# Performance work log

Measured on AMD Instinct MI355X. Metric: run time of the kernel, lower is better.

Reference implementation:

```python
import jax, jax.numpy as jnp
import numpy as np

C = 192          # channels
HEADS = 4        # num_heads
HID = int(C * 2.66)  # 510, GDFN hidden features
B, H, W = 2, 192, 192


def setup_inputs() -> dict:
    key = jax.random.key(0)
    ks = jax.random.split(key, 8)
    def nrm(k, shape, scale=0.02):
        return jax.random.normal(k, shape, jnp.float32) * scale
    return dict(
        x=jax.random.normal(ks[0], (B, C, H, W), jnp.float32),
        qkv_w=nrm(ks[1], (3 * C, C)),
        qkv_b=jnp.zeros((3 * C,), jnp.float32),
        qkv_dw_w=nrm(ks[2], (3 * C, 1, 3, 3)),
        qkv_dw_b=jnp.zeros((3 * C,), jnp.float32),
        attn_out_w=nrm(ks[3], (C, C)),
        attn_out_b=jnp.zeros((C,), jnp.float32),
        temperature=jnp.ones((HEADS, 1, 1), jnp.float32),
        proj_in_w=nrm(ks[4], (2 * HID, C)),
        proj_in_b=jnp.zeros((2 * HID,), jnp.float32),
        dw_w=nrm(ks[5], (2 * HID, 1, 3, 3)),
        dw_b=jnp.zeros((2 * HID,), jnp.float32),
        proj_out_w=nrm(ks[6], (C, HID)),
        proj_out_b=jnp.zeros((C,), jnp.float32),
    )


def _instance_norm(x):
    # torch InstanceNorm2d default: affine=False, eps=1e-5, biased var over spatial dims
    m = x.mean(axis=(2, 3), keepdims=True)
    v = ((x - m) ** 2).mean(axis=(2, 3), keepdims=True)
    return (x - m) * jax.lax.rsqrt(v + 1e-5)


def _conv1x1(x, w, b):
    return jnp.einsum('oc,bchw->bohw', w, x) + b[None, :, None, None]


def _dwconv3x3(x, w, b):
    y = jax.lax.conv_general_dilated(
        x, w, window_strides=(1, 1), padding='SAME',
        feature_group_count=x.shape[1],
        dimension_numbers=('NCHW', 'OIHW', 'NCHW'))
    return y + b[None, :, None, None]


def _l2norm(x, eps=1e-12):
    # F.normalize(dim=-1)
    n = jnp.sqrt(jnp.sum(x * x, axis=-1, keepdims=True))
    return x / jnp.maximum(n, eps)


def reference(x, qkv_w, qkv_b, qkv_dw_w, qkv_dw_b, attn_out_w, attn_out_b,
              temperature, proj_in_w, proj_in_b, dw_w, dw_b, proj_out_w, proj_out_b):
    b, c, h, w = x.shape
    hw = h * w
    dh = c // HEADS  # per-head channel dim

    # --- transposed (channel) attention branch ---
    y = _instance_norm(x)
    qkv = _dwconv3x3(_conv1x1(y, qkv_w, qkv_b), qkv_dw_w, qkv_dw_b)  # [b, 3c, h, w]
    q, k, v = jnp.split(qkv, 3, axis=1)
    q = _l2norm(q.reshape(b, HEADS, dh, hw))  # normalize along spatial dim
    k = _l2norm(k.reshape(b, HEADS, dh, hw))
    v = v.reshape(b, HEADS, dh, hw)
    attn = jnp.einsum('bhcn,bhdn->bhcd', q, k) * temperature  # small [b,heads,dh,dh]
    attn = jax.nn.softmax(attn, axis=-1)
    out = jnp.einsum('bhcd,bhdn->bhcn', attn, v).reshape(b, c, h, w)
    x = x + _conv1x1(out, attn_out_w, attn_out_b)

    # --- gated depthwise FFN (GDFN) branch ---
    y = _instance_norm(x)
    y = _dwconv3x3(_conv1x1(y, proj_in_w, proj_in_b), dw_w, dw_b)  # [b, 2*HID, h, w]
    y1, y2 = jnp.split(y, 2, axis=1)
    y = _conv1x1(jax.nn.gelu(y1, approximate=False) * y2, proj_out_w, proj_out_b)
    return x + y
```

## Files before the change

kernel.cpp:

```cpp
#include <hip/hip_runtime.h>
#include <math.h>

#define HW 36864
#define IMGW 192

typedef unsigned short u16;
typedef __attribute__((ext_vector_type(8))) short short8;
typedef __attribute__((ext_vector_type(8))) unsigned short ushort8;
typedef __attribute__((ext_vector_type(16))) float f32x16;

__device__ __forceinline__ float b2f(u16 u){ return __uint_as_float(((unsigned)u)<<16); }
__device__ __forceinline__ u16 f2b(float f){
    unsigned u = __float_as_uint(f);
    return (u16)((u + 0x7FFFu + ((u>>16)&1u)) >> 16);
}
__device__ __forceinline__ int perm1020(int m){ return (m&1) ? 510+(m>>1) : (m>>1); }
__device__ __forceinline__ int rot2(int ch){ return ((ch<<2)|(ch>>3)) & 31; }
__device__ __forceinline__ float gelu_exact(float x){
    return 0.5f * x * (1.f + erff(x * 0.70710678118654752f));
}
__device__ __forceinline__ void gll16(const u16* g, u16* l){
    __builtin_amdgcn_global_load_lds(
        (const __attribute__((address_space(1))) void*)g,
        (__attribute__((address_space(3))) void*)l, 16, 0, 0);
}

__global__ __launch_bounds__(256)
void zero_k(float* __restrict__ p, int n)
{
    int i = blockIdx.x * 256 + threadIdx.x;
    if (i < n) p[i] = 0.f;
}

__global__ __launch_bounds__(192)
void prep1_k(const float* __restrict__ w, const float* __restrict__ b,
             const float4* __restrict__ st, u16* __restrict__ wo, float* __restrict__ bo)
{
    int m = blockIdx.x, k = threadIdx.x, bz = blockIdx.y;
    st += (long)bz*192; wo += (long)bz*640*192; bo += (long)bz*640;
    float4 s = st[k];
    float wv = (m < 576) ? w[(long)m*192 + k] * s.y : 0.f;
    u16 wb = f2b(wv);
    wo[(long)m*192 + k] = wb;
    float contrib = b2f(wb) * s.x;
    for (int off = 32; off; off >>= 1) contrib += __shfl_down(contrib, off);
    __shared__ float red[3];
    if ((k & 63) == 0) red[k >> 6] = contrib;
    __syncthreads();
    if (k == 0) bo[m] = ((m < 576) ? b[m] : 0.f) - (red[0] + red[1] + red[2]);
}

__global__ __launch_bounds__(192)
void prep2_k(const float* __restrict__ w, const float* __restrict__ b,
             const float* __restrict__ s2m, const float* __restrict__ s2r,
             u16* __restrict__ wo, float* __restrict__ bo)
{
    int m = blockIdx.x, k = threadIdx.x, bz = blockIdx.y;
    s2m += (long)bz*192; s2r += (long)bz*192; wo += (long)bz*1024*192; bo += (long)bz*1024;
    bool valid = (m < 1020);
    int src = valid ? perm1020(m) : 0;
    float wv = valid ? w[(long)src*192 + k] * s2r[k] : 0.f;
    u16 wb = f2b(wv);
    wo[(long)m*192 + k] = wb;
    float contrib = b2f(wb) * s2m[k];
    for (int off = 32; off; off >>= 1) contrib += __shfl_down(contrib, off);
    __shared__ float red[3];
    if ((k & 63) == 0) red[k >> 6] = contrib;
    __syncthreads();
    if (k == 0) bo[m] = (valid ? b[src] : 0.f) - (red[0] + red[1] + red[2]);
}

__global__ __launch_bounds__(256)
void prep3_k(const float* __restrict__ w, u16* __restrict__ wo)
{
    int m = blockIdx.x;
    for (int k = threadIdx.x; k < 512; k += 256)
        wo[(long)m*512 + k] = (k < 510) ? f2b(w[(long)m*510 + k]) : (u16)0;
}

__global__ __launch_bounds__(256)
void tn_k(const float* __restrict__ xb, u16* __restrict__ xt,
          float* __restrict__ ps, float* __restrict__ pq)
{
    const int bz = blockIdx.z;
    xb += (long)bz*192*HW; xt += (long)bz*HW*192;
    ps += (long)bz*576*192; pq += (long)bz*576*192;
    __shared__ float L[64 * 196];
    long n0 = (long)blockIdx.x * 64;
    int tid = threadIdx.x;
    #pragma unroll
    for (int i = 0; i < 48; ++i) {
        int idx = tid + i*256;
        int n = idx & 63, c = idx >> 6;
        L[n*196 + c] = xb[(long)c*HW + n0 + n];
    }
    __syncthreads();
    if (tid < 192) {
        float s = 0.f, q = 0.f;
        #pragma unroll 8
        for (int n = 0; n < 64; ++n) { float f = L[n*196 + tid]; s += f; q = fmaf(f, f, q); }
        ps[blockIdx.x*192 + tid] = s;
        pq[blockIdx.x*192 + tid] = q;
    }
    #pragma unroll
    for (int i = 0; i < 6; ++i) {
        int idx = tid + i*256;
        int oc = idx % 24, n = idx / 24;
        ushort8 v;
        #pragma unroll
        for (int e = 0; e < 8; ++e) v[e] = f2b(L[n*196 + oc*8 + e]);
        *reinterpret_cast<ushort8*>(xt + (n0+n)*192 + oc*8) = v;
    }
}

__global__ __launch_bounds__(64)
void fin1b_k(const float* __restrict__ ps, const float* __restrict__ pq, float4* __restrict__ st)
{
    int c = blockIdx.x, t = threadIdx.x, bz = blockIdx.y;
    ps += (long)bz*576*192; pq += (long)bz*576*192; st += (long)bz*192;
    float s = 0.f, q = 0.f;
    for (int b = t; b < 576; b += 64) { s += ps[b*192 + c]; q += pq[b*192 + c]; }
    for (int off = 32; off; off >>= 1) { s += __shfl_down(s, off); q += __shfl_down(q, off); }
    if (t == 0) {
        float mean = s / (float)HW;
        float var  = q / (float)HW - mean*mean;
        st[c] = make_float4(mean, rsqrtf(var + 1e-5f), 0.f, 0.f);
    }
}

__global__ __launch_bounds__(64)
void fin2b_k(const float* __restrict__ ps, const float* __restrict__ pq,
             float* __restrict__ m, float* __restrict__ r)
{
    int c = blockIdx.x, t = threadIdx.x, bz = blockIdx.y;
    ps += (long)bz*288*192; pq += (long)bz*288*192; m += (long)bz*192; r += (long)bz*192;
    float s = 0.f, q = 0.f;
    for (int b = t; b < 288; b += 64) { s += ps[b*192 + c]; q += pq[b*192 + c]; }
    for (int off = 32; off; off >>= 1) { s += __shfl_down(s, off); q += __shfl_down(q, off); }
    if (t == 0) {
        float mean = s / (float)HW;
        float var  = q / (float)HW - mean*mean;
        m[c] = mean;
        r[c] = rsqrtf(var + 1e-5f);
    }
}

template<int BM, int RESID, bool OUTT>
__global__ __launch_bounds__(256)
void gemm_k(const u16* __restrict__ W, int Kpad, int K64, long wstr,
            const u16* __restrict__ B, int brs, long bstr,
            const float* __restrict__ bias, int biasstr,
            const u16* __restrict__ Rs, long rstr,
            u16* __restrict__ outA, int ors, long ostr, int Mout,
            float* __restrict__ outT, long otstr,
            float* __restrict__ p2s, float* __restrict__ p2q)
{
    constexpr int MR  = BM / 64;
    constexpr int OLS = BM + 8;
    constexpr int L_MAIN = 8192 + BM*64;
    constexpr int L_OUT  = 128*OLS;
    constexpr int LDSU = L_MAIN > L_OUT ? L_MAIN : L_OUT;
    __shared__ u16 lds[LDSU];
    __shared__ float cws[256], cwq[256];
    u16* Xl = lds;
    u16* Wl = lds + 8192;

    const int bz = blockIdx.z;
    W += (long)bz*wstr; B += (long)bz*bstr; bias += (long)bz*biasstr;
    if (RESID) Rs += (long)bz*rstr;
    if (!OUTT) outA += (long)bz*ostr; else outT += (long)bz*otstr;

    const int tid = threadIdx.x;
    const int m0 = blockIdx.x * BM;
    const long nn0 = (long)blockIdx.y * 128;
    const int ln = tid & 63, wv = tid >> 6;
    const int wn = (wv >> 1) * 64;
    const int wm = (wv & 1) * (BM/2);
    const int l31 = ln & 31, l5 = ln >> 5;

    const u16* Bb = B + nn0*(long)brs;
    const u16* Wb = W + (long)m0*Kpad;

    f32x16 acc[2][MR];
    #pragma unroll
    for (int a = 0; a < 2; ++a)
        #pragma unroll
        for (int b = 0; b < MR; ++b)
            #pragma unroll
            for (int r = 0; r < 16; ++r) acc[a][b][r] = 0.f;

    for (int ks = 0; ks < K64; ++ks) {
        #pragma unroll
        for (int i = 0; i < 4; ++i) {
            int chunk = i*256 + tid;
            int row = chunk >> 3, o = chunk & 7;
            int op = o ^ ((row >> 1) & 7);
            gll16(Bb + (long)row*brs + ks*64 + op*8, Xl + chunk*8);
        }
        #pragma unroll
        for (int i = 0; i < BM/32; ++i) {
            int chunk = i*256 + tid;
            int row = chunk >> 3, o = chunk & 7;
            int op = o ^ ((row >> 1) & 7);
            gll16(Wb + (long)row*Kpad + ks*64 + op*8, Wl + chunk*8);
        }
        __syncthreads();
        #pragma unroll
        for (int k16 = 0; k16 < 4; ++k16) {
            short8 af[2];
            #pragma unroll
            for (int nr = 0; nr < 2; ++nr) {
                int row = wn + nr*32 + l31;
                int slot = (k16*2 + l5) ^ ((row >> 1) & 7);
                af[nr] = *reinterpret_cast<const short8*>(&Xl[row*64 + slot*8]);
            }
            short8 bf[MR];
            #pragma unroll
            for (int mr = 0; mr < MR; ++mr) {
                int rowm = wm + mr*32 + l31;
                int slot = (k16*2 + l5) ^ ((rowm >> 1) & 7);
                bf[mr] = *reinterpret_cast<const short8*>(&Wl[rowm*64 + slot*8]);
            }
            #pragma unroll
            for (int nr = 0; nr < 2; ++nr)
                #pragma unroll
                for (int mr = 0; mr < MR; ++mr)
                    acc[nr][mr] = __builtin_amdgcn_mfma_f32_32x32x16_bf16(af[nr], bf[mr], acc[nr][mr], 0, 0, 0);
        }
        __syncthreads();
    }
    float bsv[MR];
    #pragma unroll
    for (int mr = 0; mr < MR; ++mr)
        bsv[mr] = bias[m0 + wm + mr*32 + l31];
    u16* Ol = lds;
    #pragma unroll
    for (int nr = 0; nr < 2; ++nr)
        #pragma unroll
        for (int mr = 0; mr < MR; ++mr)
            #pragma unroll
            for (int reg = 0; reg < 16; ++reg) {
                int r32 = (reg & 3) + 8*(reg >> 2) + 4*l5;
                int grow = wn + nr*32 + r32;
                int gcol = wm + mr*32 + l31;
                float val = acc[nr][mr][reg] + bsv[mr];
                if (RESID == 2)
                    val += b2f(Rs[(nn0 + grow)*192 + m0 + gcol]);
                Ol[grow*OLS + gcol] = f2b(val);
            }
    __syncthreads();
    if (!OUTT) {
        constexpr int SPR = BM/8;
        float ls[8] = {0,0,0,0,0,0,0,0}, lq[8] = {0,0,0,0,0,0,0,0};
        #pragma unroll
        for (int i = 0; i < 128*SPR/256; ++i) {
            int idx = tid + i*256;
            int row = idx / SPR, sl = idx % SPR;
            if (m0 + sl*8 >= Mout) continue;
            ushort8 v = *reinterpret_cast<const ushort8*>(&Ol[row*OLS + sl*8]);
            if (RESID == 1) {
                ushort8 rv = *reinterpret_cast<const ushort8*>(Rs + (nn0+row)*(long)ors + m0 + sl*8);
                #pragma unroll
                for (int e = 0; e < 8; ++e) {
                    v[e] = f2b(b2f(v[e]) + b2f(rv[e]));
                    float vv = b2f(v[e]);
                    ls[e] += vv; lq[e] = fmaf(vv, vv, lq[e]);
                }
            }
            *reinterpret_cast<ushort8*>(outA + (nn0+row)*(long)ors + m0 + sl*8) = v;
        }
        if (RESID == 1) {
            #pragma unroll
            for (int e = 0; e < 8; ++e) {
                float s = ls[e], q = lq[e];
                s += __shfl_xor(s, 8);  q += __shfl_xor(q, 8);
                s += __shfl_xor(s, 16); q += __shfl_xor(q, 16);
                s += __shfl_xor(s, 32); q += __shfl_xor(q, 32);
                if (ln < 8) { cws[wv*64 + ln*8 + e] = s; cwq[wv*64 + ln*8 + e] = q; }
            }
            __syncthreads();
            if (tid < 64) {
                float s = cws[tid] + cws[64+tid] + cws[128+tid] + cws[192+tid];
                float q = cwq[tid] + cwq[64+tid] + cwq[128+tid] + cwq[192+tid];
                p2s[(long)bz*288*192 + blockIdx.y*192 + m0 + tid] = s;
                p2q[(long)bz*288*192 + blockIdx.y*192 + m0 + tid] = q;
            }
        }
    } else {
        int m = tid >> 2, ng = tid & 3;
        float* orow = outT + (long)(m0 + m)*HW + nn0 + ng*32;
        #pragma unroll
        for (int i = 0; i < 32; i += 4) {
            float4 o;
            o.x = b2f(Ol[(ng*32+i+0)*OLS + m]);
            o.y = b2f(Ol[(ng*32+i+1)*OLS + m]);
            o.z = b2f(Ol[(ng*32+i+2)*OLS + m]);
            o.w = b2f(Ol[(ng*32+i+3)*OLS + m]);
            *reinterpret_cast<float4*>(orow + i) = o;
        }
    }
}

__global__ __launch_bounds__(256)
void dwconv_k(const u16* __restrict__ in, const float* __restrict__ dww,
              const float* __restrict__ dwb, u16* __restrict__ vbuf,
              u16* __restrict__ qkT, float* __restrict__ nacc, const u16* __restrict__ zp)
{
    const int bz = blockIdx.z;
    in += (long)bz*HW*576; vbuf += (long)bz*HW*192;
    qkT += (long)bz*384*HW; nacc += (long)bz*384;
    __shared__ u16 T[10*34*32];
    __shared__ float wl[32][9];
    __shared__ float bl[32];
    __shared__ float nsum[32];
    const int tid = threadIdx.x;
    const int cg = blockIdx.y;
    const int ty = blockIdx.x / 6, tx = blockIdx.x % 6;
    const int y0 = ty*8, x0 = tx*32;
    const bool isv = (cg >= 12);
    const int cbase = cg*32;

    for (int i = tid; i < 288; i += 256) wl[i/9][i%9] = dww[cbase*9 + i];
    if (tid < 32) { bl[tid] = dwb[cbase + tid]; nsum[tid] = 0.f; }
    #pragma unroll
    for (int it = 0; it < 6; ++it) {
        int i = it*256 + tid;
        if (i < 1360) {
            int r = i / 136;
            int rem = i - r*136;
            int c = rem >> 2, o = rem & 3;
            int gy = y0 - 1 + r, gx = x0 - 1 + c;
            const u16* src = ((unsigned)gy < 192u && (unsigned)gx < 192u)
                ? in + ((long)gy*192 + gx)*576 + cbase + o*8 : zp;
            gll16(src, T + i*8);
        }
    }
    __syncthreads();

    const int o2 = tid & 3, xc = (tid >> 2) & 31, yh = tid >> 7;
    float wr[9][8], bs[8];
    #pragma unroll
    for (int j = 0; j < 9; ++j)
        #pragma unroll
        for (int e = 0; e < 8; ++e) wr[j][e] = wl[o2*8+e][j];
    #pragma unroll
    for (int e = 0; e < 8; ++e) bs[e] = bl[o2*8+e];

    float acc[4][8];
    #pragma unroll
    for (int yy = 0; yy < 4; ++yy)
        #pragma unroll
        for (int e = 0; e < 8; ++e) acc[yy][e] = bs[e];
    #pragma unroll
    for (int r = 0; r < 6; ++r) {
        const int rr = yh*4 + r;
        float f[3][8];
        #pragma unroll
        for (int dx = 0; dx < 3; ++dx) {
            ushort8 v = *reinterpret_cast<const ushort8*>(&T[(rr*34 + xc+dx)*32 + o2*8]);
            #pragma unroll
            for (int e = 0; e < 8; ++e) f[dx][e] = b2f(v[e]);
        }
        #pragma unroll
        for (int yy = 0; yy < 4; ++yy) {
            const int dy = r - yy;
            if (dy < 0 || dy > 2) continue;
            #pragma unroll
            for (int dx = 0; dx < 3; ++dx)
                #pragma unroll
                for (int e = 0; e < 8; ++e)
                    acc[yy][e] = fmaf(f[dx][e], wr[dy*3+dx][e], acc[yy][e]);
        }
    }
    float sq[8] = {0.f,0.f,0.f,0.f,0.f,0.f,0.f,0.f};
    ushort8 ov[4];
    #pragma unroll
    for (int yy = 0; yy < 4; ++yy) {
        int y = yh*4 + yy;
        #pragma unroll
        for (int e = 0; e < 8; ++e) { float a = acc[yy][e]; ov[yy][e] = f2b(a); sq[e] = fmaf(a, a, sq[e]); }
        if (isv)
            *reinterpret_cast<ushort8*>(vbuf + ((long)(y0+y)*192 + x0+xc)*192 + (cg-12)*32 + o2*8) = ov[yy];
    }
    if (!isv) {
        #pragma unroll
        for (int e = 0; e < 8; ++e) {
            float s = sq[e];
            s += __shfl_xor(s, 4); s += __shfl_xor(s, 8);
            s += __shfl_xor(s, 16); s += __shfl_xor(s, 32);
            if ((tid & 63) < 4) atomicAdd(&nsum[o2*8 + e], s);
        }
        __syncthreads();
        if (tid < 32) atomicAdd(&nacc[cbase + tid], nsum[tid]);
        #pragma unroll
        for (int yy = 0; yy < 4; ++yy) {
            int y = yh*4 + yy;
            #pragma unroll
            for (int e = 0; e < 8; ++e) {
                int ch = o2*8 + e;
                int slot = y*4 + (xc >> 3);
                T[ch*256 + ((slot ^ rot2(ch)) & 31)*8 + (xc & 7)] = ov[yy][e];
            }
        }
        __syncthreads();
        #pragma unroll
        for (int i = 0; i < 4; ++i) {
            int idx = i*256 + tid;
            int ch = idx >> 5, slot = idx & 31;
            ushort8 v = *reinterpret_cast<const ushort8*>(&T[ch*256 + ((slot ^ rot2(ch)) & 31)*8]);
            int yy2 = slot >> 2, sx = slot & 3;
            *reinterpret_cast<ushort8*>(qkT + (long)(cbase+ch)*HW + (long)(y0+yy2)*192 + x0 + sx*8) = v;
        }
    }
}

__global__ __launch_bounds__(256)
void attnscore_k(const u16* __restrict__ qkT, float* __restrict__ apart)
{
    const int bz = blockIdx.z;
    qkT += (long)bz*384*HW; apart += (long)bz*72*9216;
    __shared__ u16 lds[8192];
    u16* Al = lds;
    u16* Bl = lds + 4096;
    const int tid = threadIdx.x;
    const int h = blockIdx.y;
    const long nb = (long)blockIdx.x * 512;
    const int ln = tid & 63, wv = tid >> 6;
    const int wq = (wv >> 1) * 32, wd = (wv & 1) * 32;
    const int l31 = ln & 31, l5 = ln >> 5;

    f32x16 acc;
    #pragma unroll
    for (int r = 0; r < 16; ++r) acc[r] = 0.f;

    for (int ks = 0; ks < 8; ++ks) {
        #pragma unroll
        for (int i = 0; i < 2; ++i) {
            int chunk = i*256 + tid;
            int row = chunk >> 3, o = chunk & 7;
            int op = o ^ ((row >> 1) & 7);
            int qr = h*48 + (row < 48 ? row : 0);
            gll16(qkT + (long)qr*HW + nb + ks*64 + op*8, Al + chunk*8);
        }
        #pragma unroll
        for (int i = 0; i < 2; ++i) {
            int chunk = i*256 + tid;
            int row = chunk >> 3, o = chunk & 7;
            int op = o ^ ((row >> 1) & 7);
            int kr = 192 + h*48 + (row < 48 ? row : 0);
            gll16(qkT + (long)kr*HW + nb + ks*64 + op*8, Bl + chunk*8);
        }
        __syncthreads();
        #pragma unroll
        for (int k16 = 0; k16 < 4; ++k16) {
            int rq = wq + l31;
            int sq_ = (k16*2 + l5) ^ ((rq >> 1) & 7);
            short8 af = *reinterpret_cast<const short8*>(&Al[rq*64 + sq_*8]);
            int rk = wd + l31;
            int sk = (k16*2 + l5) ^ ((rk >> 1) & 7);
            short8 bf = *reinterpret_cast<const short8*>(&Bl[rk*64 + sk*8]);
            acc = __builtin_amdgcn_mfma_f32_32x32x16_bf16(af, bf, acc, 0, 0, 0);
        }
        __syncthreads();
    }
    float* ap = apart + ((long)blockIdx.x*4 + h) * 2304;
    #pragma unroll
    for (int reg = 0; reg < 16; ++reg) {
        int c = wq + (reg & 3) + 8*(reg >> 2) + 4*l5;
        int d = wd + l31;
        if (c < 48 && d < 48) ap[c*48 + d] = acc[reg];
    }
}

__global__ __launch_bounds__(256)
void red_k(const float* __restrict__ apart, float* __restrict__ araw)
{
    const int bz = blockIdx.y;
    apart += (long)bz*72*9216; araw += (long)bz*9216;
    int idx = blockIdx.x*256 + threadIdx.x;
    float s = 0.f;
    for (int p = 0; p < 72; ++p) s += apart[(long)p*9216 + idx];
    araw[idx] = s;
}

__global__ __launch_bounds__(256)
void softmax_sm_k(const float* __restrict__ araw, const float* __restrict__ nacc,
                  const float* __restrict__ temp, float* __restrict__ ssm)
{
    const int bz = blockIdx.x;
    araw += (long)bz*9216; nacc += (long)bz*384; ssm += (long)bz*9216;
    int tid = threadIdx.x;
    if (tid >= 192) return;
    int h = tid / 48, c = tid % 48;
    float qn = fmaxf(sqrtf(nacc[h*48 + c]), 1e-12f);
    float ti = temp[h] / qn;
    const float* ar = araw + h*2304 + c*48;
    const float* nk = nacc + 192 + h*48;
    float row[48];
    float mx = -1e30f;
    #pragma unroll
    for (int d = 0; d < 48; ++d) {
        float kn = fmaxf(sqrtf(nk[d]), 1e-12f);
        row[d] = ar[d] * ti / kn;
        mx = fmaxf(mx, row[d]);
    }
    float ssum = 0.f;
    #pragma unroll
    for (int d = 0; d < 48; ++d) { float e = expf(row[d] - mx); row[d] = e; ssum += e; }
    float inv = 1.f / ssum;
    float* so = ssm + h*2304 + c*48;
    #pragma unroll
    for (int d = 0; d < 48; ++d) so[d] = row[d] * inv;
}

__global__ __launch_bounds__(256)
void w2fold_k(const float* __restrict__ ssm, const float* __restrict__ aow,
              u16* __restrict__ W2b)
{
    const int bz = blockIdx.y;
    ssm += (long)bz*9216; W2b += (long)bz*36864;
    int idx = blockIdx.x*256 + threadIdx.x;
    int o = idx / 192, col = idx % 192;
    int h = col / 48, d = col % 48;
    const float* ar = aow + (long)o*192 + h*48;
    const float* sp = ssm + h*2304 + d;
    float s = 0.f;
    #pragma unroll
    for (int c = 0; c < 48; ++c) s = fmaf(ar[c], sp[c*48], s);
    W2b[idx] = f2b(s);
}

__global__ __launch_bounds__(256)
void gate_k(const u16* __restrict__ t2h, const float* __restrict__ dww,
            const float* __restrict__ dwb, u16* __restrict__ g, int jbase,
            const u16* __restrict__ zp)
{
    const int bz = blockIdx.z;
    t2h += (long)bz*HW*512; g += (long)bz*HW*576;
    __shared__ u16 T[10*34*32];
    __shared__ float w1l[16][9], w2l[16][9];
    __shared__ float b1l[16], b2l[16];
    const int tid = threadIdx.x;
    const int cg = blockIdx.y;
    const int ty = blockIdx.x / 6, tx = blockIdx.x % 6;
    const int y0 = ty*8, x0 = tx*32;
    const int jb = jbase + cg*16;

    for (int i = tid; i < 144; i += 256) {
        int p = i/9, j = i%9;
        int gj = jb + p;
        bool ok = (gj < 510);
        w1l[p][j] = ok ? dww[(long)gj*9 + j] : 0.f;
        w2l[p][j] = ok ? dww[(long)(510+gj)*9 + j] : 0.f;
    }
    if (tid < 16) {
        int gj = jb + tid;
        bool ok = (gj < 510);
        b1l[tid] = ok ? dwb[gj] : 0.f;
        b2l[tid] = ok ? dwb[510+gj] : 0.f;
    }
    #pragma unroll
    for (int it = 0; it < 6; ++it) {
        int i = it*256 + tid;
        if (i < 1360) {
            int r = i / 136;
            int rem = i - r*136;
            int c = rem >> 2, o = rem & 3;
            int gy = y0 - 1 + r, gx = x0 - 1 + c;
            const u16* src = ((unsigned)gy < 192u && (unsigned)gx < 192u)
                ? t2h + ((long)gy*192 + gx)*512 + cg*32 + o*8 : zp;
            gll16(src, T + i*8);
        }
    }
    __syncthreads();

    const int o2 = tid & 3, xc = (tid >> 2) & 31, yh = tid >> 7;
    float w1r[4][9], w2r[4][9], b1r[4], b2r[4];
    #pragma unroll
    for (int p = 0; p < 4; ++p) {
        #pragma unroll
        for (int j = 0; j < 9; ++j) { w1r[p][j] = w1l[o2*4+p][j]; w2r[p][j] = w2l[o2*4+p][j]; }
        b1r[p] = b1l[o2*4+p]; b2r[p] = b2l[o2*4+p];
    }
    float a1[4][4], a2[4][4];
    #pragma unroll
    for (int yy = 0; yy < 4; ++yy)
        #pragma unroll
        for (int p = 0; p < 4; ++p) { a1[yy][p] = b1r[p]; a2[yy][p] = b2r[p]; }
    #pragma unroll
    for (int r = 0; r < 6; ++r) {
        const int rr = yh*4 + r;
        float f1[3][4], f2[3][4];
        #pragma unroll
        for (int dx = 0; dx < 3; ++dx) {
            ushort8 v = *reinterpret_cast<const ushort8*>(&T[(rr*34 + xc+dx)*32 + o2*8]);
            #pragma unroll
            for (int p = 0; p < 4; ++p) { f1[dx][p] = b2f(v[2*p]); f2[dx][p] = b2f(v[2*p+1]); }
        }
        #pragma unroll
        for (int yy = 0; yy < 4; ++yy) {
            const int dy = r - yy;
            if (dy < 0 || dy > 2) continue;
            #pragma unroll
            for (int dx = 0; dx < 3; ++dx)
                #pragma unroll
                for (int p = 0; p < 4; ++p) {
                    a1[yy][p] = fmaf(f1[dx][p], w1r[p][dy*3+dx], a1[yy][p]);
                    a2[yy][p] = fmaf(f2[dx][p], w2r[p][dy*3+dx], a2[yy][p]);
                }
        }
    }
    #pragma unroll
    for (int yy = 0; yy < 4; ++yy) {
        int y = yh*4 + yy;
        ushort4 ovv;
        ovv.x = f2b(gelu_exact(a1[yy][0]) * a2[yy][0]);
        ovv.y = f2b(gelu_exact(a1[yy][1]) * a2[yy][1]);
        ovv.z = f2b(gelu_exact(a1[yy][2]) * a2[yy][2]);
        ovv.w = f2b(gelu_exact(a1[yy][3]) * a2[yy][3]);
        *reinterpret_cast<ushort4*>(g + ((long)(y0+y)*192 + x0+xc)*512 + jb + o2*4) = ovv;
    }
}

extern "C" void kernel_launch(void* const* d_in, const int* in_sizes, int n_in,
                              void* d_out, int out_size, void* d_ws, size_t ws_size,
                              hipStream_t stream) {
    const float* x           = (const float*)d_in[0];
    const float* qkv_w       = (const float*)d_in[1];
    const float* qkv_bias    = (const float*)d_in[2];
    const float* qkv_dw_w    = (const float*)d_in[3];
    const float* qkv_dw_b    = (const float*)d_in[4];
    const float* attn_out_w  = (const float*)d_in[5];
    const float* attn_out_b  = (const float*)d_in[6];
    const float* temperature = (const float*)d_in[7];
    const float* proj_in_w   = (const float*)d_in[8];
    const float* proj_in_b   = (const float*)d_in[9];
    const float* dw_w        = (const float*)d_in[10];
    const float* dw_b        = (const float*)d_in[11];
    const float* proj_out_w  = (const float*)d_in[12];
    const float* proj_out_b  = (const float*)d_in[13];
    float* out = (float*)d_out;
    char* ws = (char*)d_ws;

    const bool batched = (ws_size >= 210000000ull);
    const long nb = batched ? 2 : 1;

    const long ASZ = (long)HW*192*2;
    const long CSZ = (long)HW*576*2;
    const long VSZ = (long)HW*192*2;
    const long QSZ = (long)384*HW*2;
    u16* A_   = (u16*)ws;
    u16* C_   = (u16*)(ws + nb*ASZ);
    u16* vbuf = (u16*)(ws + nb*(ASZ + CSZ));
    u16* qkT  = (u16*)(ws + nb*(ASZ + CSZ + VSZ));
    u16* E_   = vbuf;
    char* wsm = ws + nb*(ASZ + CSZ + VSZ + QSZ);
    u16* W1p = (u16*)(wsm);
    u16* W2p = (u16*)(wsm + nb*245760);
    u16* W3p = (u16*)(wsm + nb*(245760 + 393216));
    u16* W2b = (u16*)(wsm + nb*(245760 + 393216) + 196608);
    float* b1p = (float*)(wsm + nb*(245760 + 393216 + 73728) + 196608);
    float* b2p = b1p + nb*640;
    float* S_  = b2p + nb*1024;
    float* zpadf = S_;
    float* nacc  = S_ + 8;
    float* araw  = nacc + nb*384;
    float* ssm   = araw + nb*9216;
    float4* st1  = (float4*)(ssm + nb*9216);
    float* s2m   = (float*)(st1 + nb*192);
    float* s2r   = s2m + nb*192;
    float* apart = s2r + nb*192;
    float* p1s = apart;
    float* p1q = apart + nb*110592;
    float* p2s = apart;
    float* p2q = apart + nb*55296;
    const u16* zp = (const u16*)zpadf;

    const long AE = (long)HW*192;
    const long CE = (long)HW*576;
    const long VE = (long)HW*192;
    const long QE = (long)384*HW;
    const long EE = (long)HW*512;

    prep3_k<<<192, 256, 0, stream>>>(proj_out_w, W3p);

    if (batched) {
        zero_k<<<4, 256, 0, stream>>>(S_, 8 + 2*384);
        tn_k<<<dim3(576,1,2), 256, 0, stream>>>(x, A_, p1s, p1q);
        fin1b_k<<<dim3(192,2), 64, 0, stream>>>(p1s, p1q, st1);
        prep1_k<<<dim3(640,2), 192, 0, stream>>>(qkv_w, qkv_bias, st1, W1p, b1p);

        gemm_k<128,0,false><<<dim3(5,288,2), 256, 0, stream>>>(
            W1p, 192, 3, 640*192, A_, 192, AE, b1p, 640, nullptr, 0, C_, 576, CE, 576, nullptr, 0, nullptr, nullptr);
        dwconv_k<<<dim3(144,18,2), 256, 0, stream>>>(C_, qkv_dw_w, qkv_dw_b, vbuf, qkT, nacc, zp);
        attnscore_k<<<dim3(72,4,2), 256, 0, stream>>>(qkT, apart);
        red_k<<<dim3(36,2), 256, 0, stream>>>(apart, araw);
        softmax_sm_k<<<2, 256, 0, stream>>>(araw, nacc, temperature, ssm);
        w2fold_k<<<dim3(144,2), 256, 0, stream>>>(ssm, attn_out_w, W2b);
        gemm_k<64,1,false><<<dim3(3,288,2), 256, 0, stream>>>(
            W2b, 192, 3, 36864, vbuf, 192, VE, attn_out_b, 0, A_, AE, A_, 192, AE, 192, nullptr, 0, p2s, p2q);

        fin2b_k<<<dim3(192,2), 64, 0, stream>>>(p2s, p2q, s2m, s2r);
        prep2_k<<<dim3(1024,2), 192, 0, stream>>>(proj_in_w, proj_in_b, s2m, s2r, W2p, b2p);

        gemm_k<128,0,false><<<dim3(4,288,2), 256, 0, stream>>>(
            W2p, 192, 3, 1024*192, A_, 192, AE, b2p, 1024, nullptr, 0, E_, 512, EE, 512, nullptr, 0, nullptr, nullptr);
        gate_k<<<dim3(144,16,2), 256, 0, stream>>>(E_, dw_w, dw_b, C_, 0, zp);
        gemm_k<128,0,false><<<dim3(4,288,2), 256, 0, stream>>>(
            W2p + (long)512*192, 192, 3, 1024*192, A_, 192, AE, b2p + 512, 1024, nullptr, 0, E_, 512, EE, 512, nullptr, 0, nullptr, nullptr);
        gate_k<<<dim3(144,16,2), 256, 0, stream>>>(E_, dw_w, dw_b, C_, 256, zp);

        gemm_k<64,2,true><<<dim3(3,288,2), 256, 0, stream>>>(
            W3p, 512, 8, 0, C_, 512, CE, proj_out_b, 0, A_, AE, nullptr, 0, 0, 192, out, (long)192*HW, nullptr, nullptr);
    } else {
        for (int b = 0; b < 2; ++b) {
            const float* xb = x + (long)b * 192 * HW;
            float* outb = out + (long)b * 192 * HW;

            zero_k<<<2, 256, 0, stream>>>(S_, 8 + 384);
            tn_k<<<dim3(576,1,1), 256, 0, stream>>>(xb, A_, p1s, p1q);
            fin1b_k<<<dim3(192,1), 64, 0, stream>>>(p1s, p1q, st1);
            prep1_k<<<dim3(640,1), 192, 0, stream>>>(qkv_w, qkv_bias, st1, W1p, b1p);

            gemm_k<128,0,false><<<dim3(5,288,1), 256, 0, stream>>>(
                W1p, 192, 3, 0, A_, 192, 0, b1p, 0, nullptr, 0, C_, 576, 0, 576, nullptr, 0, nullptr, nullptr);
            dwconv_k<<<dim3(144,18,1), 256, 0, stream>>>(C_, qkv_dw_w, qkv_dw_b, vbuf, qkT, nacc, zp);
            attnscore_k<<<dim3(72,4,1), 256, 0, stream>>>(qkT, apart);
            red_k<<<dim3(36,1), 256, 0, stream>>>(apart, araw);
            softmax_sm_k<<<1, 256, 0, stream>>>(araw, nacc, temperature, ssm);
            w2fold_k<<<dim3(144,1), 256, 0, stream>>>(ssm, attn_out_w, W2b);
            gemm_k<64,1,false><<<dim3(3,288,1), 256, 0, stream>>>(
                W2b, 192, 3, 0, vbuf, 192, 0, attn_out_b, 0, A_, 0, A_, 192, 0, 192, nullptr, 0, p2s, p2q);

            fin2b_k<<<dim3(192,1), 64, 0, stream>>>(p2s, p2q, s2m, s2r);
            prep2_k<<<dim3(1024,1), 192, 0, stream>>>(proj_in_w, proj_in_b, s2m, s2r, W2p, b2p);

            gemm_k<128,0,false><<<dim3(4,288,1), 256, 0, stream>>>(
                W2p, 192, 3, 0, A_, 192, 0, b2p, 0, nullptr, 0, E_, 512, 0, 512, nullptr, 0, nullptr, nullptr);
            gate_k<<<dim3(144,16,1), 256, 0, stream>>>(E_, dw_w, dw_b, C_, 0, zp);
            gemm_k<128,0,false><<<dim3(4,288,1), 256, 0, stream>>>(
                W2p + (long)512*192, 192, 3, 0, A_, 192, 0, b2p + 512, 0, nullptr, 0, E_, 512, 0, 512, nullptr, 0, nullptr, nullptr);
            gate_k<<<dim3(144,16,1), 256, 0, stream>>>(E_, dw_w, dw_b, C_, 256, zp);

            gemm_k<64,2,true><<<dim3(3,288,1), 256, 0, stream>>>(
                W3p, 512, 8, 0, C_, 512, 0, proj_out_b, 0, A_, 0, nullptr, 0, 0, 192, outb, 0, nullptr, nullptr);
        }
    }
}
```

Measured before the change: 395.9 us.

## Emit QKV GEMM output channel-major and split depthwise conv into q/k and v kernels

The QKV projection GEMM gains a third epilogue mode that writes its bf16 output channel-planar (channel-major over HW) instead of pixel-major. This lets the q/k depthwise conv work on whole planes row by row, writing planar q/k directly and accumulating L2 norms, so the in-LDS transpose of the old fused dwconv kernel goes away. V gets its own kernel that reads planar input and transposes back to the pixel-major layout the next GEMM consumes. The cost is an extra launch, a strided transposed LDS write in the GEMM epilogue, and a v kernel that works on only 8 channels per block with scalar math.

New measurement: 402.5 us. No clear change (+1.7%).

```diff
diff --git a/kernel.cpp b/kernel.cpp
--- a/kernel.cpp
+++ b/kernel.cpp
@@ -15,7 +15,6 @@
     return (u16)((u + 0x7FFFu + ((u>>16)&1u)) >> 16);
 }
 __device__ __forceinline__ int perm1020(int m){ return (m&1) ? 510+(m>>1) : (m>>1); }
-__device__ __forceinline__ int rot2(int ch){ return ((ch<<2)|(ch>>3)) & 31; }
 __device__ __forceinline__ float gelu_exact(float x){
     return 0.5f * x * (1.f + erff(x * 0.70710678118654752f));
 }
@@ -145,7 +144,7 @@
     }
 }
 
-template<int BM, int RESID, bool OUTT>
+template<int BM, int RESID, int OUTT>
 __global__ __launch_bounds__(256)
 void gemm_k(const u16* __restrict__ W, int Kpad, int K64, long wstr,
             const u16* __restrict__ B, int brs, long bstr,
@@ -156,9 +155,9 @@
             float* __restrict__ p2s, float* __restrict__ p2q)
 {
     constexpr int MR  = BM / 64;
-    constexpr int OLS = BM + 8;
+    constexpr int OLS = (OUTT==0) ? (BM+8) : 130;
     constexpr int L_MAIN = 8192 + BM*64;
-    constexpr int L_OUT  = 128*OLS;
+    constexpr int L_OUT  = (OUTT==0) ? 128*OLS : BM*130;
     constexpr int LDSU = L_MAIN > L_OUT ? L_MAIN : L_OUT;
     __shared__ u16 lds[LDSU];
     __shared__ float cws[256], cwq[256];
@@ -168,7 +167,7 @@
     const int bz = blockIdx.z;
     W += (long)bz*wstr; B += (long)bz*bstr; bias += (long)bz*biasstr;
     if (RESID) Rs += (long)bz*rstr;
-    if (!OUTT) outA += (long)bz*ostr; else outT += (long)bz*otstr;
+    if (OUTT==1) outT += (long)bz*otstr; else outA += (long)bz*ostr;
 
     const int tid = threadIdx.x;
     const int m0 = blockIdx.x * BM;
@@ -246,10 +245,11 @@
                 float val = acc[nr][mr][reg] + bsv[mr];
                 if (RESID == 2)
                     val += b2f(Rs[(nn0 + grow)*192 + m0 + gcol]);
-                Ol[grow*OLS + gcol] = f2b(val);
+                if (OUTT == 0) Ol[grow*OLS + gcol] = f2b(val);
+                else           Ol[gcol*130 + grow] = f2b(val);
             }
     __syncthreads();
-    if (!OUTT) {
+    if (OUTT == 0) {
         constexpr int SPR = BM/8;
         float ls[8] = {0,0,0,0,0,0,0,0}, lq[8] = {0,0,0,0,0,0,0,0};
         #pragma unroll
@@ -286,132 +286,140 @@
                 p2q[(long)bz*288*192 + blockIdx.y*192 + m0 + tid] = q;
             }
         }
-    } else {
+    } else if (OUTT == 1) {
         int m = tid >> 2, ng = tid & 3;
         float* orow = outT + (long)(m0 + m)*HW + nn0 + ng*32;
         #pragma unroll
-        for (int i = 0; i < 32; i += 4) {
-            float4 o;
-            o.x = b2f(Ol[(ng*32+i+0)*OLS + m]);
-            o.y = b2f(Ol[(ng*32+i+1)*OLS + m]);
-            o.z = b2f(Ol[(ng*32+i+2)*OLS + m]);
-            o.w = b2f(Ol[(ng*32+i+3)*OLS + m]);
-            *reinterpret_cast<float4*>(orow + i) = o;
-        }
-    }
-}
-
-__global__ __launch_bounds__(256)
-void dwconv_k(const u16* __restrict__ in, const float* __restrict__ dww,
-              const float* __restrict__ dwb, u16* __restrict__ vbuf,
-              u16* __restrict__ qkT, float* __restrict__ nacc, const u16* __restrict__ zp)
+        for (int i = 0; i < 32; i += 8) {
+            ushort8 v = *reinterpret_cast<const ushort8*>(&Ol[m*130 + ng*32 + i]);
+            float4 o1 = make_float4(b2f(v[0]), b2f(v[1]), b2f(v[2]), b2f(v[3]));
+            float4 o2 = make_float4(b2f(v[4]), b2f(v[5]), b2f(v[6]), b2f(v[7]));
+            *reinterpret_cast<float4*>(orow + i)     = o1;
+            *reinterpret_cast<float4*>(orow + i + 4) = o2;
+        }
+    } else {
+        int m = tid >> 1, ng = tid & 1;
+        if (m0 + m < Mout) {
+            u16* orow = outA + (long)(m0 + m)*HW + nn0 + ng*64;
+            #pragma unroll
+            for (int i = 0; i < 64; i += 8)
+                *reinterpret_cast<ushort8*>(orow + i) =
+                    *reinterpret_cast<const ushort8*>(&Ol[m*130 + ng*64 + i]);
+        }
+    }
+}
+
+__global__ __launch_bounds__(256)
+void dwq_k(const u16* __restrict__ t1P, const float* __restrict__ dww,
+           const float* __restrict__ dwb, u16* __restrict__ qkP,
+           float* __restrict__ nacc, const u16* __restrict__ zp)
 {
     const int bz = blockIdx.z;
-    in += (long)bz*HW*576; vbuf += (long)bz*HW*192;
-    qkT += (long)bz*384*HW; nacc += (long)bz*384;
-    __shared__ u16 T[10*34*32];
-    __shared__ float wl[32][9];
-    __shared__ float bl[32];
-    __shared__ float nsum[32];
+    t1P += (long)bz*HW*576; qkP += (long)bz*384*(long)HW; nacc += (long)bz*384;
+    const int plane = blockIdx.y;
+    const int y0 = blockIdx.x * 16;
+    __shared__ u16 Ts[18*192];
+    __shared__ float wq[10];
+    __shared__ float wsum[4];
     const int tid = threadIdx.x;
+    if (tid < 9) wq[tid] = dww[plane*9 + tid];
+    if (tid == 9) wq[9] = dwb[plane];
+    const u16* pl = t1P + (long)plane*HW;
+    for (int i = tid; i < 432; i += 256) {
+        int r = i / 24, c8 = i - r*24;
+        int gy = y0 - 1 + r;
+        const u16* src = ((unsigned)gy < 192u) ? pl + gy*192 + c8*8 : zp;
+        gll16(src, Ts + i*8);
+    }
+    __syncthreads();
+    float w[9];
+    #pragma unroll
+    for (int j = 0; j < 9; ++j) w[j] = wq[j];
+    const float bias = wq[9];
+    float sq = 0.f;
+    for (int cc = tid; cc < 384; cc += 256) {
+        int y = cc / 24, x8 = cc - y*24;
+        float a[8];
+        #pragma unroll
+        for (int e = 0; e < 8; ++e) a[e] = bias;
+        #pragma unroll
+        for (int dy = 0; dy < 3; ++dy) {
+            const u16* R = &Ts[(y+dy)*192];
+            ushort8 mid = *reinterpret_cast<const ushort8*>(&R[x8*8]);
+            ushort8 lft = x8       ? *reinterpret_cast<const ushort8*>(&R[x8*8-8]) : (ushort8)0;
+            ushort8 rgt = (x8<23)  ? *reinterpret_cast<const ushort8*>(&R[x8*8+8]) : (ushort8)0;
+            float v[10];
+            v[0] = b2f(lft[7]);
+            #pragma unroll
+            for (int e = 0; e < 8; ++e) v[1+e] = b2f(mid[e]);
+            v[9] = b2f(rgt[0]);
+            #pragma unroll
+            for (int dx = 0; dx < 3; ++dx)
+                #pragma unroll
+                for (int e = 0; e < 8; ++e)
+                    a[e] = fmaf(v[e+dx], w[dy*3+dx], a[e]);
+        }
+        ushort8 ov;
+        #pragma unroll
+        for (int e = 0; e < 8; ++e) { ov[e] = f2b(a[e]); sq = fmaf(a[e], a[e], sq); }
+        *reinterpret_cast<ushort8*>(qkP + (long)plane*HW + (y0+y)*192 + x8*8) = ov;
+    }
+    for (int off = 32; off; off >>= 1) sq += __shfl_down(sq, off);
+    if ((tid & 63) == 0) wsum[tid >> 6] = sq;
+    __syncthreads();
+    if (tid == 0) atomicAdd(&nacc[plane], wsum[0]+wsum[1]+wsum[2]+wsum[3]);
+}
+
+__global__ __launch_bounds__(256)
+void dwv_k(const u16* __restrict__ t1P, const float* __restrict__ dww,
+           const float* __restrict__ dwb, u16* __restrict__ vbuf,
+           const u16* __restrict__ zp)
+{
+    const int bz = blockIdx.z;
+    t1P += (long)bz*HW*576; vbuf += (long)bz*HW*192;
     const int cg = blockIdx.y;
     const int ty = blockIdx.x / 6, tx = blockIdx.x % 6;
     const int y0 = ty*8, x0 = tx*32;
-    const bool isv = (cg >= 12);
-    const int cbase = cg*32;
-
-    for (int i = tid; i < 288; i += 256) wl[i/9][i%9] = dww[cbase*9 + i];
-    if (tid < 32) { bl[tid] = dwb[cbase + tid]; nsum[tid] = 0.f; }
-    #pragma unroll
-    for (int it = 0; it < 6; ++it) {
-        int i = it*256 + tid;
-        if (i < 1360) {
-            int r = i / 136;
-            int rem = i - r*136;
-            int c = rem >> 2, o = rem & 3;
-            int gy = y0 - 1 + r, gx = x0 - 1 + c;
-            const u16* src = ((unsigned)gy < 192u && (unsigned)gx < 192u)
-                ? in + ((long)gy*192 + gx)*576 + cbase + o*8 : zp;
-            gll16(src, T + i*8);
-        }
-    }
-    __syncthreads();
-
-    const int o2 = tid & 3, xc = (tid >> 2) & 31, yh = tid >> 7;
-    float wr[9][8], bs[8];
-    #pragma unroll
-    for (int j = 0; j < 9; ++j)
-        #pragma unroll
-        for (int e = 0; e < 8; ++e) wr[j][e] = wl[o2*8+e][j];
-    #pragma unroll
-    for (int e = 0; e < 8; ++e) bs[e] = bl[o2*8+e];
-
-    float acc[4][8];
-    #pragma unroll
-    for (int yy = 0; yy < 4; ++yy)
-        #pragma unroll
-        for (int e = 0; e < 8; ++e) acc[yy][e] = bs[e];
-    #pragma unroll
-    for (int r = 0; r < 6; ++r) {
-        const int rr = yh*4 + r;
-        float f[3][8];
-        #pragma unroll
-        for (int dx = 0; dx < 3; ++dx) {
-            ushort8 v = *reinterpret_cast<const ushort8*>(&T[(rr*34 + xc+dx)*32 + o2*8]);
-            #pragma unroll
-            for (int e = 0; e < 8; ++e) f[dx][e] = b2f(v[e]);
-        }
-        #pragma unroll
-        for (int yy = 0; yy < 4; ++yy) {
-            const int dy = r - yy;
-            if (dy < 0 || dy > 2) continue;
-            #pragma unroll
-            for (int dx = 0; dx < 3; ++dx)
-                #pragma unroll
-                for (int e = 0; e < 8; ++e)
-                    acc[yy][e] = fmaf(f[dx][e], wr[dy*3+dx][e], acc[yy][e]);
-        }
-    }
-    float sq[8] = {0.f,0.f,0.f,0.f,0.f,0.f,0.f,0.f};
-    ushort8 ov[4];
-    #pragma unroll
-    for (int yy = 0; yy < 4; ++yy) {
-        int y = yh*4 + yy;
-        #pragma unroll
-        for (int e = 0; e < 8; ++e) { float a = acc[yy][e]; ov[yy][e] = f2b(a); sq[e] = fmaf(a, a, sq[e]); }
-        if (isv)
-            *reinterpret_cast<ushort8*>(vbuf + ((long)(y0+y)*192 + x0+xc)*192 + (cg-12)*32 + o2*8) = ov[yy];
-    }
-    if (!isv) {
-        #pragma unroll
-        for (int e = 0; e < 8; ++e) {
-            float s = sq[e];
-            s += __shfl_xor(s, 4); s += __shfl_xor(s, 8);
-            s += __shfl_xor(s, 16); s += __shfl_xor(s, 32);
-            if ((tid & 63) < 4) atomicAdd(&nsum[o2*8 + e], s);
-        }
-        __syncthreads();
-        if (tid < 32) atomicAdd(&nacc[cbase + tid], nsum[tid]);
-        #pragma unroll
-        for (int yy = 0; yy < 4; ++yy) {
-            int y = yh*4 + yy;
-            #pragma unroll
-            for (int e = 0; e < 8; ++e) {
-                int ch = o2*8 + e;
-                int slot = y*4 + (xc >> 3);
-                T[ch*256 + ((slot ^ rot2(ch)) & 31)*8 + (xc & 7)] = ov[yy][e];
-            }
-        }
-        __syncthreads();
-        #pragma unroll
-        for (int i = 0; i < 4; ++i) {
-            int idx = i*256 + tid;
-            int ch = idx >> 5, slot = idx & 31;
-            ushort8 v = *reinterpret_cast<const ushort8*>(&T[ch*256 + ((slot ^ rot2(ch)) & 31)*8]);
-            int yy2 = slot >> 2, sx = slot & 3;
-            *reinterpret_cast<ushort8*>(qkT + (long)(cbase+ch)*HW + (long)(y0+yy2)*192 + x0 + sx*8) = v;
-        }
-    }
+    __shared__ u16 Tv[8*10*48];
+    __shared__ u16 T2[256*8];
+    __shared__ float wl[8][9];
+    __shared__ float bl[8];
+    const int tid = threadIdx.x;
+    for (int i = tid; i < 72; i += 256) wl[i/9][i%9] = dww[(long)(384 + cg*8 + i/9)*9 + i%9];
+    if (tid < 8) bl[tid] = dwb[384 + cg*8 + tid];
+    for (int i = tid; i < 480; i += 256) {
+        int o = i / 60; int rem = i - o*60;
+        int r = rem / 6, c8 = rem - r*6;
+        int gy = y0 - 1 + r;
+        int gx0 = x0 - 8 + c8*8;
+        const u16* src = ((unsigned)gy < 192u && (unsigned)gx0 <= 184u)
+            ? t1P + (long)(384 + cg*8 + o)*HW + gy*192 + gx0 : zp;
+        gll16(src, Tv + i*8);
+    }
+    __syncthreads();
+    const int o = tid >> 5, xc = tid & 31;
+    float w[9];
+    #pragma unroll
+    for (int j = 0; j < 9; ++j) w[j] = wl[o][j];
+    const float bias = bl[o];
+    const u16* base = &Tv[o*480];
+    #pragma unroll
+    for (int y = 0; y < 8; ++y) {
+        float a = bias;
+        #pragma unroll
+        for (int dy = 0; dy < 3; ++dy) {
+            const u16* R = base + (y+dy)*48 + xc + 7;
+            a = fmaf(b2f(R[0]), w[dy*3+0], a);
+            a = fmaf(b2f(R[1]), w[dy*3+1], a);
+            a = fmaf(b2f(R[2]), w[dy*3+2], a);
+        }
+        T2[(y*32 + xc)*8 + o] = f2b(a);
+    }
+    __syncthreads();
+    const int px = tid;
+    const int yy = px >> 5, xx = px & 31;
+    *reinterpret_cast<ushort8*>(vbuf + ((long)(y0+yy)*192 + x0+xx)*192 + cg*8) =
+        *reinterpret_cast<const ushort8*>(&T2[px*8]);
 }
 
 __global__ __launch_bounds__(256)
@@ -652,7 +660,7 @@
     u16* A_   = (u16*)ws;
     u16* C_   = (u16*)(ws + nb*ASZ);
     u16* vbuf = (u16*)(ws + nb*(ASZ + CSZ));
-    u16* qkT  = (u16*)(ws + nb*(ASZ + CSZ + VSZ));
+    u16* qkP  = (u16*)(ws + nb*(ASZ + CSZ + VSZ));
     u16* E_   = vbuf;
     char* wsm = ws + nb*(ASZ + CSZ + VSZ + QSZ);
     u16* W1p = (u16*)(wsm);
@@ -679,7 +687,6 @@
     const long AE = (long)HW*192;
     const long CE = (long)HW*576;
     const long VE = (long)HW*192;
-    const long QE = (long)384*HW;
     const long EE = (long)HW*512;
 
     prep3_k<<<192, 256, 0, stream>>>(proj_out_w, W3p);
@@ -690,27 +697,28 @@
         fin1b_k<<<dim3(192,2), 64, 0, stream>>>(p1s, p1q, st1);
         prep1_k<<<dim3(640,2), 192, 0, stream>>>(qkv_w, qkv_bias, st1, W1p, b1p);
 
-        gemm_k<128,0,false><<<dim3(5,288,2), 256, 0, stream>>>(
-            W1p, 192, 3, 640*192, A_, 192, AE, b1p, 640, nullptr, 0, C_, 576, CE, 576, nullptr, 0, nullptr, nullptr);
-        dwconv_k<<<dim3(144,18,2), 256, 0, stream>>>(C_, qkv_dw_w, qkv_dw_b, vbuf, qkT, nacc, zp);
-        attnscore_k<<<dim3(72,4,2), 256, 0, stream>>>(qkT, apart);
+        gemm_k<128,0,2><<<dim3(5,288,2), 256, 0, stream>>>(
+            W1p, 192, 3, 640*192, A_, 192, AE, b1p, 640, nullptr, 0, C_, 0, CE, 576, nullptr, 0, nullptr, nullptr);
+        dwq_k<<<dim3(12,384,2), 256, 0, stream>>>(C_, qkv_dw_w, qkv_dw_b, qkP, nacc, zp);
+        dwv_k<<<dim3(144,24,2), 256, 0, stream>>>(C_, qkv_dw_w, qkv_dw_b, vbuf, zp);
+        attnscore_k<<<dim3(72,4,2), 256, 0, stream>>>(qkP, apart);
         red_k<<<dim3(36,2), 256, 0, stream>>>(apart, araw);
         softmax_sm_k<<<2, 256, 0, stream>>>(araw, nacc, temperature, ssm);
         w2fold_k<<<dim3(144,2), 256, 0, stream>>>(ssm, attn_out_w, W2b);
-        gemm_k<64,1,false><<<dim3(3,288,2), 256, 0, stream>>>(
+        gemm_k<64,1,0><<<dim3(3,288,2), 256, 0, stream>>>(
             W2b, 192, 3, 36864, vbuf, 192, VE, attn_out_b, 0, A_, AE, A_, 192, AE, 192, nullptr, 0, p2s, p2q);
 
         fin2b_k<<<dim3(192,2), 64, 0, stream>>>(p2s, p2q, s2m, s2r);
         prep2_k<<<dim3(1024,2), 192, 0, stream>>>(proj_in_w, proj_in_b, s2m, s2r, W2p, b2p);
 
-        gemm_k<128,0,false><<<dim3(4,288,2), 256, 0, stream>>>(
+        gemm_k<128,0,0><<<dim3(4,288,2), 256, 0, stream>>>(
             W2p, 192, 3, 1024*192, A_, 192, AE, b2p, 1024, nullptr, 0, E_, 512, EE, 512, nullptr, 0, nullptr, nullptr);
         gate_k<<<dim3(144,16,2), 256, 0, stream>>>(E_, dw_w, dw_b, C_, 0, zp);
-        gemm_k<128,0,false><<<dim3(4,288,2), 256, 0, stream>>>(
+        gemm_k<128,0,0><<<dim3(4,288,2), 256, 0, stream>>>(
             W2p + (long)512*192, 192, 3, 1024*192, A_, 192, AE, b2p + 512, 1024, nullptr, 0, E_, 512, EE, 512, nullptr, 0, nullptr, nullptr);
         gate_k<<<dim3(144,16,2), 256, 0, stream>>>(E_, dw_w, dw_b, C_, 256, zp);
 
-        gemm_k<64,2,true><<<dim3(3,288,2), 256, 0, stream>>>(
+        gemm_k<64,2,1><<<dim3(3,288,2), 256, 0, stream>>>(
             W3p, 512, 8, 0, C_, 512, CE, proj_out_b, 0, A_, AE, nullptr, 0, 0, 192, out, (long)192*HW, nullptr, nullptr);
     } else {
         for (int b = 0; b < 2; ++b) {
@@ -722,27 +730,28 @@
             fin1b_k<<<dim3(192,1), 64, 0, stream>>>(p1s, p1q, st1);
             prep1_k<<<dim3(640,1), 192, 0, stream>>>(qkv_w, qkv_bias, st1, W1p, b1p);
 
-            gemm_k<128,0,false><<<dim3(5,288,1), 256, 0, stream>>>(
-                W1p, 192, 3, 0, A_, 192, 0, b1p, 0, nullptr, 0, C_, 576, 0, 576, nullptr, 0, nullptr, nullptr);
-            dwconv_k<<<dim3(144,18,1), 256, 0, stream>>>(C_, qkv_dw_w, qkv_dw_b, vbuf, qkT, nacc, zp);
-            attnscore_k<<<dim3(72,4,1), 256, 0, stream>>>(qkT, apart);
+            gemm_k<128,0,2><<<dim3(5,288,1), 256, 0, stream>>>(
+                W1p, 192, 3, 0, A_, 192, 0, b1p, 0, nullptr, 0, C_, 0, 0, 576, nullptr, 0, nullptr, nullptr);
+            dwq_k<<<dim3(12,384,1), 256, 0, stream>>>(C_, qkv_dw_w, qkv_dw_b, qkP, nacc, zp);
+            dwv_k<<<dim3(144,24,1), 256, 0, stream>>>(C_, qkv_dw_w, qkv_dw_b, vbuf, zp);
+            attnscore_k<<<dim3(72,4,1), 256, 0, stream>>>(qkP, apart);
             red_k<<<dim3(36,1), 256, 0, stream>>>(apart, araw);
             softmax_sm_k<<<1, 256, 0, stream>>>(araw, nacc, temperature, ssm);
             w2fold_k<<<dim3(144,1), 256, 0, stream>>>(ssm, attn_out_w, W2b);
-            gemm_k<64,1,false><<<dim3(3,288,1), 256, 0, stream>>>(
+            gemm_k<64,1,0><<<dim3(3,288,1), 256, 0, stream>>>(
                 W2b, 192, 3, 0, vbuf, 192, 0, attn_out_b, 0, A_, 0, A_, 192, 0, 192, nullptr, 0, p2s, p2q);
 
             fin2b_k<<<dim3(192,1), 64, 0, stream>>>(p2s, p2q, s2m, s2r);
             prep2_k<<<dim3(1024,1), 192, 0, stream>>>(proj_in_w, proj_in_b, s2m, s2r, W2p, b2p);
 
-            gemm_k<128,0,false><<<dim3(4,288,1), 256, 0, stream>>>(
+            gemm_k<128,0,0><<<dim3(4,288,1), 256, 0, stream>>>(
                 W2p, 192, 3, 0, A_, 192, 0, b2p, 0, nullptr, 0, E_, 512, 0, 512, nullptr, 0, nullptr, nullptr);
             gate_k<<<dim3(144,16,1), 256, 0, stream>>>(E_, dw_w, dw_b, C_, 0, zp);
-            gemm_k<128,0,false><<<dim3(4,288,1), 256, 0, stream>>>(
+            gemm_k<128,0,0><<<dim3(4,288,1), 256, 0, stream>>>(
                 W2p + (long)512*192, 192, 3, 0, A_, 192, 0, b2p + 512, 0, nullptr, 0, E_, 512, 0, 512, nullptr, 0, nullptr, nullptr);
             gate_k<<<dim3(144,16,1), 256, 0, stream>>>(E_, dw_w, dw_b, C_, 256, zp);
 
-            gemm_k<64,2,true><<<dim3(3,288,1), 256, 0, stream>>>(
+            gemm_k<64,2,1><<<dim3(3,288,1), 256, 0, stream>>>(
                 W3p, 512, 8, 0, C_, 512, 0, proj_out_b, 0, A_, 0, nullptr, 0, 0, 192, outb, 0, nullptr, nullptr);
         }
     }
```
